# Optimization experiments

Measured on AMD Instinct MI355X. Metric: run time of the kernel, lower is better.

Reference implementation:

```python
import jax, jax.numpy as jnp
import numpy as np

N_NODES, F_IN, HID = 50000, 128, 64
N_EDGES = 400000


def _mean_agg(x, ei, n):
    # mean of src features over incoming edges per dst node
    src, dst = ei[0], ei[1]
    s = jax.ops.segment_sum(x[src], dst, num_segments=n)
    cnt = jax.ops.segment_sum(jnp.ones((ei.shape[1],), x.dtype), dst, num_segments=n)
    return s / jnp.maximum(cnt, 1.0)[:, None]


def _conv(x, ei, Wd, Ws, Wu):
    # HeteroGNNConv: mean-aggregate, then lin_dst(x_dst) || lin_src(aggr) -> lin_update
    agg = _mean_agg(x, ei, x.shape[0])
    comb = jnp.concatenate([x @ Wd.T, agg @ Ws.T], axis=-1)  # [N, 2H]
    return comb @ Wu.T


def _bn(x, g, b):
    # BatchNorm1d training-mode, eps=1 (as in the source), biased variance
    m = x.mean(axis=0)
    v = jnp.var(x, axis=0)
    return (x - m) * jax.lax.rsqrt(v + 1.0) * g + b


def setup_inputs() -> dict:
    key = jax.random.key(0)
    ks = jax.random.split(key, 20)
    d = {}
    d['node_feature'] = jax.random.normal(ks[0], (N_NODES, F_IN), dtype=jnp.float32)
    d['edge_index0'] = jax.random.randint(ks[1], (2, N_EDGES), 0, N_NODES, dtype=jnp.int32)
    d['edge_index1'] = jax.random.randint(ks[2], (2, N_EDGES), 0, N_NODES, dtype=jnp.int32)
    i = 3
    for layer, fin in (('l1', F_IN), ('l2', HID)):
        for t in ('t0', 't1'):
            d[f'{layer}{t}_Wd'] = jax.random.normal(ks[i], (HID, fin), dtype=jnp.float32) / np.sqrt(fin); i += 1
            d[f'{layer}{t}_Ws'] = jax.random.normal(ks[i], (HID, fin), dtype=jnp.float32) / np.sqrt(fin); i += 1
            d[f'{layer}{t}_Wu'] = jax.random.normal(ks[i], (HID, 2 * HID), dtype=jnp.float32) / np.sqrt(2 * HID); i += 1
    d['bn1_g'] = jnp.ones((HID,), jnp.float32)
    d['bn1_b'] = jnp.zeros((HID,), jnp.float32)
    d['bn2_g'] = jnp.ones((HID,), jnp.float32)
    d['bn2_b'] = jnp.zeros((HID,), jnp.float32)
    return d


def reference(node_feature, edge_index0, edge_index1,
              l1t0_Wd, l1t0_Ws, l1t0_Wu, l1t1_Wd, l1t1_Ws, l1t1_Wu,
              l2t0_Wd, l2t0_Ws, l2t0_Wu, l2t1_Wd, l2t1_Ws, l2t1_Wu,
              bn1_g, bn1_b, bn2_g, bn2_b):
    x = node_feature
    # layer 1: two message-type convs, mean cross-type aggregation, BN, LeakyReLU
    h = 0.5 * (_conv(x, edge_index0, l1t0_Wd, l1t0_Ws, l1t0_Wu)
               + _conv(x, edge_index1, l1t1_Wd, l1t1_Ws, l1t1_Wu))
    x = jax.nn.leaky_relu(_bn(h, bn1_g, bn1_b), negative_slope=0.01)
    # layer 2
    h = 0.5 * (_conv(x, edge_index0, l2t0_Wd, l2t0_Ws, l2t0_Wu)
               + _conv(x, edge_index1, l2t1_Wd, l2t1_Ws, l2t1_Wu))
    x = jax.nn.leaky_relu(_bn(h, bn2_g, bn2_b), negative_slope=0.01)
    # edge embeddings: [src || dst] per edge, concatenated over edge types
    e0 = jnp.concatenate([x[edge_index0[0]], x[edge_index0[1]]], axis=1)
    e1 = jnp.concatenate([x[edge_index1[0]], x[edge_index1[1]]], axis=1)
    return jnp.concatenate([e0, e1], axis=0)  # [2E, 2H]
```

## Files before the change

### kernel.cpp

```cpp
#include <hip/hip_runtime.h>
#include <math.h>


typedef float f32x4 __attribute__((ext_vector_type(4)));
typedef float f32x2 __attribute__((ext_vector_type(2)));
typedef short bf16x8 __attribute__((ext_vector_type(8)));
typedef unsigned short u16x4 __attribute__((ext_vector_type(4)));

#define NB_SCAN 64

static __device__ __forceinline__ unsigned short f2bf(float f) {
  unsigned int u = __builtin_bit_cast(unsigned int, f);
  unsigned int r = (u + 0x7FFFu + ((u >> 16) & 1u)) >> 16;
  return (unsigned short)r;
}
static __device__ __forceinline__ float bfl(unsigned int u) {
  return __builtin_bit_cast(float, u << 16);
}
static __device__ __forceinline__ float bfh(unsigned int u) {
  return __builtin_bit_cast(float, u & 0xFFFF0000u);
}

__global__ void zero_cnt(int* __restrict__ cnt0, int* __restrict__ cnt1,
                         float* __restrict__ s1, float* __restrict__ s2, int N) {
  int g = blockIdx.x * 256 + threadIdx.x;
  if (g < N) { cnt0[g] = 0; cnt1[g] = 0; }
  if (g < 256) { s1[g] = 0.f; s2[g] = 0.f; }
}

__global__ void prep_kernel(const float* __restrict__ x, unsigned short* __restrict__ xb,
                            int n4, int cvtB,
                            const float* __restrict__ Wd10, const float* __restrict__ Ws10,
                            const float* __restrict__ Wu10, const float* __restrict__ Wd11,
                            const float* __restrict__ Ws11, const float* __restrict__ Wu11,
                            unsigned short* __restrict__ Wfb1,
                            const float* __restrict__ Wd20, const float* __restrict__ Ws20,
                            const float* __restrict__ Wu20, const float* __restrict__ Wd21,
                            const float* __restrict__ Ws21, const float* __restrict__ Wu21,
                            unsigned short* __restrict__ Wfb2) {
  int b = blockIdx.x;
  if (b < cvtB) {
    int g = b * 256 + threadIdx.x;
    if (g >= n4) return;
    f32x4 v = ((const f32x4*)x)[g];
    u16x4 o;
#pragma unroll
    for (int j = 0; j < 4; ++j) o[j] = f2bf(v[j]);
    ((u16x4*)xb)[g] = o;
    return;
  }
  const float *Wd0, *Ws0, *Wu0, *Wd1, *Ws1, *Wu1;
  unsigned short* Wfb;
  int K, gid;
  if (b < cvtB + 96) {
    Wd0 = Wd10; Ws0 = Ws10; Wu0 = Wu10; Wd1 = Wd11; Ws1 = Ws11; Wu1 = Wu11;
    Wfb = Wfb1; K = 128;
    gid = (b - cvtB) * 256 + threadIdx.x;
  } else {
    Wd0 = Wd20; Ws0 = Ws20; Wu0 = Wu20; Wd1 = Wd21; Ws1 = Ws21; Wu1 = Wu21;
    Wfb = Wfb2; K = 64;
    gid = (b - cvtB - 96) * 256 + threadIdx.x;
  }
  if (gid >= 192 * K) return;
  int i = gid / K, j = gid - i * K;
  float s = 0.f;
  if (i < 64) {
#pragma unroll 4
    for (int k = 0; k < 64; ++k)
      s += Wu0[i * 128 + k] * Wd0[k * K + j] + Wu1[i * 128 + k] * Wd1[k * K + j];
  } else if (i < 128) {
    int ii = i - 64;
#pragma unroll 4
    for (int k = 0; k < 64; ++k) s += Wu0[ii * 128 + 64 + k] * Ws0[k * K + j];
  } else {
    int ii = i - 128;
#pragma unroll 4
    for (int k = 0; k < 64; ++k) s += Wu1[ii * 128 + 64 + k] * Ws1[k * K + j];
  }
  Wfb[gid] = f2bf(0.5f * s);
}

__global__ void count_both(const int* __restrict__ dst0, const int* __restrict__ dst1,
                           int* __restrict__ cnt0, int* __restrict__ cnt1, int E, int eg) {
  int b = blockIdx.x;
  bool t1 = b >= eg;
  int e = (t1 ? b - eg : b) * 256 + threadIdx.x;
  if (e >= E) return;
  if (t1) atomicAdd(&cnt1[dst1[e]], 1);
  else atomicAdd(&cnt0[dst0[e]], 1);
}

__global__ __launch_bounds__(256) void scanA(const int* __restrict__ cnt0,
                                             const int* __restrict__ cnt1,
                                             int* __restrict__ bsum, int N, int chunk) {
  int b = blockIdx.x;
  const int* cnt = (b < NB_SCAN) ? cnt0 : cnt1;
  int lb = (b < NB_SCAN) ? b : b - NB_SCAN;
  int lo = lb * chunk, hi = min(lo + chunk, N);
  int s = 0;
  for (int i = lo + threadIdx.x; i < hi; i += 256) s += cnt[i];
  __shared__ int red[256];
  red[threadIdx.x] = s;
  __syncthreads();
  for (int off = 128; off > 0; off >>= 1) {
    if (threadIdx.x < off) red[threadIdx.x] += red[threadIdx.x + off];
    __syncthreads();
  }
  if (threadIdx.x == 0) bsum[b] = red[0];
}

__global__ void scanB(const int* __restrict__ bsum, int* __restrict__ bbase) {
  __shared__ int l[2 * NB_SCAN];
  int t = threadIdx.x;
  int v0 = bsum[t];
  l[t] = v0;
  __syncthreads();
  for (int off = 1; off < NB_SCAN; off <<= 1) {
    int v = l[t];
    if ((t & (NB_SCAN - 1)) >= off) v += l[t - off];
    __syncthreads();
    l[t] = v;
    __syncthreads();
  }
  bbase[t] = l[t] - v0;
}

__global__ __launch_bounds__(256) void scanC(const int* __restrict__ cnt0,
                                             const int* __restrict__ cnt1,
                                             const int* __restrict__ bbase,
                                             int* __restrict__ base0, int* __restrict__ base1,
                                             int N, int chunk, int E) {
  int b = blockIdx.x;
  const int* cnt = (b < NB_SCAN) ? cnt0 : cnt1;
  int* base = (b < NB_SCAN) ? base0 : base1;
  int lb = (b < NB_SCAN) ? b : b - NB_SCAN;
  int lo = lb * chunk, hi = min(lo + chunk, N);
  int t = threadIdx.x;
  int v[4];
  int ls = 0;
  int i0 = lo + t * 4;
#pragma unroll
  for (int j = 0; j < 4; ++j) {
    v[j] = (i0 + j < hi) ? cnt[i0 + j] : 0;
    ls += v[j];
  }
  __shared__ int l[256];
  l[t] = ls;
  __syncthreads();
  for (int off = 1; off < 256; off <<= 1) {
    int x = l[t];
    if (t >= off) x += l[t - off];
    __syncthreads();
    l[t] = x;
    __syncthreads();
  }
  int run = bbase[b] + l[t] - ls;
#pragma unroll
  for (int j = 0; j < 4; ++j) {
    if (i0 + j < hi) base[i0 + j] = run;
    run += v[j];
  }
  if (t == 0 && lb == NB_SCAN - 1) base[N] = E;
}

__global__ void fill_both(const int* __restrict__ src0, const int* __restrict__ dst0,
                          const int* __restrict__ base0, int* __restrict__ cnt0,
                          int* __restrict__ csr0,
                          const int* __restrict__ src1, const int* __restrict__ dst1,
                          const int* __restrict__ base1, int* __restrict__ cnt1,
                          int* __restrict__ csr1, int E, int eg) {
  int b = blockIdx.x;
  bool t1 = b >= eg;
  int e = (t1 ? b - eg : b) * 256 + threadIdx.x;
  if (e >= E) return;
  const int* src = t1 ? src1 : src0;
  const int* dst = t1 ? dst1 : dst0;
  const int* base = t1 ? base1 : base0;
  int* cnt = t1 ? cnt1 : cnt0;
  int* csr = t1 ? csr1 : csr0;
  int d = dst[e];
  int p = atomicSub(&cnt[d], 1) - 1;
  csr[base[d] + p] = src[e];
}

template <int K>
__global__ __launch_bounds__(256) void mm_mfma(const unsigned short* __restrict__ xb,
                                               const unsigned short* __restrict__ Wfb,
                                               float* __restrict__ h,
                                               unsigned short* __restrict__ P0,
                                               unsigned short* __restrict__ P1, int N) {
  constexpr int NKS = K / 32;
  int tid = threadIdx.x;
  int l = tid & 63;
  int wv = tid >> 6;
  int lr = l & 15;
  int lj = l >> 4;
  int brow = blockIdx.x * 64;
  int wcol = wv * 48;

  bf16x8 B[3 * NKS];
#pragma unroll
  for (int ct = 0; ct < 3; ++ct)
#pragma unroll
    for (int ks = 0; ks < NKS; ++ks) {
      int col = wcol + ct * 16 + lr;
      B[ct * NKS + ks] = *(const bf16x8*)&Wfb[(size_t)col * K + ks * 32 + lj * 8];
    }

  f32x4 acc[4][3];
#pragma unroll
  for (int rt = 0; rt < 4; ++rt)
#pragma unroll
    for (int ct = 0; ct < 3; ++ct) acc[rt][ct] = (f32x4){0.f, 0.f, 0.f, 0.f};

#pragma unroll
  for (int ks = 0; ks < NKS; ++ks) {
    bf16x8 A[4];
#pragma unroll
    for (int rt = 0; rt < 4; ++rt) {
      int row = brow + rt * 16 + lr;
      if (row >= N) row = N - 1;
      A[rt] = *(const bf16x8*)&xb[(size_t)row * K + ks * 32 + lj * 8];
    }
#pragma unroll
    for (int rt = 0; rt < 4; ++rt)
#pragma unroll
      for (int ct = 0; ct < 3; ++ct)
        acc[rt][ct] =
            __builtin_amdgcn_mfma_f32_16x16x32_bf16(A[rt], B[ct * NKS + ks], acc[rt][ct], 0, 0, 0);
  }

#pragma unroll
  for (int rt = 0; rt < 4; ++rt)
#pragma unroll
    for (int ct = 0; ct < 3; ++ct) {
      int gct = (wcol >> 4) + ct;
      int sel = gct >> 2;
      int c0 = (gct & 3) * 16 + lr;
#pragma unroll
      for (int r = 0; r < 4; ++r) {
        int row = brow + rt * 16 + lj * 4 + r;
        if (row < N) {
          if (sel == 0) h[(size_t)row * 64 + c0] = acc[rt][ct][r];
          else if (sel == 1) P0[(size_t)row * 64 + c0] = f2bf(acc[rt][ct][r]);
          else P1[(size_t)row * 64 + c0] = f2bf(acc[rt][ct][r]);
        }
      }
    }
}

__global__ void agg_kernel(float* __restrict__ h, const unsigned short* __restrict__ P0,
                           const unsigned short* __restrict__ P1,
                           const int* __restrict__ csr0, const int* __restrict__ base0,
                           const int* __restrict__ csr1, const int* __restrict__ base1,
                           int N) {
  int gid = blockIdx.x * blockDim.x + threadIdx.x;
  int w = gid >> 5, c = gid & 31;
  if (w >= N) return;
  int co = 2 * c;
  float a0 = 0.f, a1 = 0.f;
  int b0 = base0[w], e0 = base0[w + 1];
  for (int i = b0; i < e0; ++i) {
    unsigned int u = *(const unsigned int*)&P0[(size_t)csr0[i] * 64 + co];
    a0 += bfl(u);
    a1 += bfh(u);
  }
  float i0 = 1.0f / fmaxf((float)(e0 - b0), 1.0f);
  float s0 = a0 * i0, s1 = a1 * i0;
  a0 = 0.f; a1 = 0.f;
  int b1 = base1[w], e1 = base1[w + 1];
  for (int i = b1; i < e1; ++i) {
    unsigned int u = *(const unsigned int*)&P1[(size_t)csr1[i] * 64 + co];
    a0 += bfl(u);
    a1 += bfh(u);
  }
  float i1 = 1.0f / fmaxf((float)(e1 - b1), 1.0f);
  s0 += a0 * i1;
  s1 += a1 * i1;
  f32x2* hp = (f32x2*)&h[(size_t)w * 64 + co];
  f32x2 hv = *hp;
  hv.x += s0;
  hv.y += s1;
  *hp = hv;
}

__global__ __launch_bounds__(256) void bnstats_kernel(const float* __restrict__ h,
                                                      float* __restrict__ stats, int N) {
  int tid = threadIdx.x;
  int c = tid & 63;
  int part = tid >> 6;
  float s = 0.f, s2 = 0.f;
  for (int r = blockIdx.x * 4 + part; r < N; r += gridDim.x * 4) {
    float v = h[(size_t)r * 64 + c];
    s += v;
    s2 += v * v;
  }
  __shared__ float red[512];
  red[tid] = s;
  red[256 + tid] = s2;
  __syncthreads();
  if (part == 0) {
    s = red[c] + red[64 + c] + red[128 + c] + red[192 + c];
    s2 = red[256 + c] + red[256 + 64 + c] + red[256 + 128 + c] + red[256 + 192 + c];
    atomicAdd(&stats[c], s);
    atomicAdd(&stats[64 + c], s2);
  }
}

__global__ void bnfinal_kernel(float* __restrict__ stats, const float* __restrict__ g,
                               const float* __restrict__ b, float invN) {
  int c = threadIdx.x;
  if (c >= 64) return;
  float m = stats[c] * invN;
  float v = stats[64 + c] * invN - m * m;
  float a = g[c] * rsqrtf(v + 1.0f);
  stats[128 + c] = a;
  stats[192 + c] = b[c] - m * a;
}

__global__ void bnapply_kernel(const float* __restrict__ h, const float* __restrict__ stats,
                               unsigned short* __restrict__ xo, int N) {
  int gid = blockIdx.x * blockDim.x + threadIdx.x;
  if (gid >= N * 16) return;
  f32x4 v = ((const f32x4*)h)[gid];
  int c = (gid & 15) * 4;
  const float* a = stats + 128;
  const float* bb = stats + 192;
  u16x4 o;
#pragma unroll
  for (int j = 0; j < 4; ++j) {
    float t = fmaf(a[c + j], v[j], bb[c + j]);
    o[j] = f2bf(fmaxf(t, 0.01f * t));
  }
  ((u16x4*)xo)[gid] = o;
}

__global__ void gather_kernel(const unsigned short* __restrict__ xc,
                              const int* __restrict__ src0, const int* __restrict__ dst0,
                              const int* __restrict__ src1, const int* __restrict__ dst1,
                              float* __restrict__ out, int E) {
  int gid = blockIdx.x * blockDim.x + threadIdx.x;
  int total = 2 * E * 32;
  if (gid >= total) return;
  int row = gid >> 5, q = gid & 31;
  int e, s, d;
  if (row < E) {
    e = row; s = src0[e]; d = dst0[e];
  } else {
    e = row - E; s = src1[e]; d = dst1[e];
  }
  int node = (q < 16) ? s : d;
  int qq = q & 15;
  u16x4 v = *(const u16x4*)&xc[(size_t)node * 64 + qq * 4];
  f32x4 o;
#pragma unroll
  for (int j = 0; j < 4; ++j) o[j] = bfl((unsigned int)v[j]);
  __builtin_nontemporal_store(o, (f32x4*)out + gid);
}

extern "C" void kernel_launch(void* const* d_in, const int* in_sizes, int n_in,
                              void* d_out, int out_size, void* d_ws, size_t ws_size,
                              hipStream_t stream) {
  const float* x0 = (const float*)d_in[0];
  const int* ei0 = (const int*)d_in[1];
  const int* ei1 = (const int*)d_in[2];
  const float* bn1_g = (const float*)d_in[15];
  const float* bn1_b = (const float*)d_in[16];
  const float* bn2_g = (const float*)d_in[17];
  const float* bn2_b = (const float*)d_in[18];

  const int N = in_sizes[0] / 128;
  const int E = in_sizes[1] / 2;
  const int *src0 = ei0, *dst0 = ei0 + E;
  const int *src1 = ei1, *dst1 = ei1 + E;

  char* wsb = (char*)d_ws;
  size_t off = 0;
  auto alloc = [&](size_t bytes) {
    char* p = wsb + off;
    off = (off + bytes + 255) & ~(size_t)255;
    return (void*)p;
  };
  unsigned short* Wfb1 = (unsigned short*)alloc(192 * 128 * 2);
  unsigned short* Wfb2 = (unsigned short*)alloc(192 * 64 * 2);
  float* stats1 = (float*)alloc(256 * 4);
  float* stats2 = (float*)alloc(256 * 4);
  int* bsum = (int*)alloc(2 * NB_SCAN * 4);
  int* bbase = (int*)alloc(2 * NB_SCAN * 4);
  int* cnt0 = (int*)alloc((size_t)N * 4);
  int* cnt1 = (int*)alloc((size_t)N * 4);
  int* base0 = (int*)alloc(((size_t)N + 1) * 4);
  int* base1 = (int*)alloc(((size_t)N + 1) * 4);
  int* csr0 = (int*)alloc((size_t)E * 4);
  int* csr1 = (int*)alloc((size_t)E * 4);
  unsigned short* xb = (unsigned short*)alloc((size_t)N * 128 * 2);
  float* h = (float*)alloc((size_t)N * 64 * 4);
  float* h2 = (float*)alloc((size_t)N * 64 * 4);
  unsigned short* P0 = (unsigned short*)alloc((size_t)N * 64 * 2);
  unsigned short* P1 = (unsigned short*)alloc((size_t)N * 64 * 2);
  unsigned short* xcb = (unsigned short*)alloc((size_t)N * 64 * 2);
  unsigned short* xc2 = (unsigned short*)alloc((size_t)N * 64 * 2);

  const float invN = 1.0f / (float)N;
  const int eg = (E + 255) / 256;
  const int chunk = (N + NB_SCAN - 1) / NB_SCAN;
  const int cvtB = (N * 32 + 255) / 256;

  zero_cnt<<<(N + 255) / 256, 256, 0, stream>>>(cnt0, cnt1, stats1, stats2, N);
  prep_kernel<<<cvtB + 96 + 48, 256, 0, stream>>>(
      x0, xb, N * 32, cvtB,
      (const float*)d_in[3], (const float*)d_in[4], (const float*)d_in[5],
      (const float*)d_in[6], (const float*)d_in[7], (const float*)d_in[8], Wfb1,
      (const float*)d_in[9], (const float*)d_in[10], (const float*)d_in[11],
      (const float*)d_in[12], (const float*)d_in[13], (const float*)d_in[14], Wfb2);
  count_both<<<2 * eg, 256, 0, stream>>>(dst0, dst1, cnt0, cnt1, E, eg);
  scanA<<<2 * NB_SCAN, 256, 0, stream>>>(cnt0, cnt1, bsum, N, chunk);
  scanB<<<1, 2 * NB_SCAN, 0, stream>>>(bsum, bbase);
  scanC<<<2 * NB_SCAN, 256, 0, stream>>>(cnt0, cnt1, bbase, base0, base1, N, chunk, E);
  fill_both<<<2 * eg, 256, 0, stream>>>(src0, dst0, base0, cnt0, csr0,
                                        src1, dst1, base1, cnt1, csr1, E, eg);

  const int mmGrid = (N + 63) / 64;
  const int aggGrid = (N * 32 + 255) / 256;

  mm_mfma<128><<<mmGrid, 256, 0, stream>>>(xb, Wfb1, h, P0, P1, N);
  agg_kernel<<<aggGrid, 256, 0, stream>>>(h, P0, P1, csr0, base0, csr1, base1, N);
  bnstats_kernel<<<256, 256, 0, stream>>>(h, stats1, N);
  bnfinal_kernel<<<1, 64, 0, stream>>>(stats1, bn1_g, bn1_b, invN);
  bnapply_kernel<<<(N * 16 + 255) / 256, 256, 0, stream>>>(h, stats1, xcb, N);

  mm_mfma<64><<<mmGrid, 256, 0, stream>>>(xcb, Wfb2, h2, P0, P1, N);
  agg_kernel<<<aggGrid, 256, 0, stream>>>(h2, P0, P1, csr0, base0, csr1, base1, N);
  bnstats_kernel<<<256, 256, 0, stream>>>(h2, stats2, N);
  bnfinal_kernel<<<1, 64, 0, stream>>>(stats2, bn2_g, bn2_b, invN);
  bnapply_kernel<<<(N * 16 + 255) / 256, 256, 0, stream>>>(h2, stats2, xc2, N);

  gather_kernel<<<(2 * E * 32 + 255) / 256, 256, 0, stream>>>(
      xc2, src0, dst0, src1, dst1, (float*)d_out, E);
}
```

Measured before the change: 367.6 us.

## Fuse fp32-to-bf16 conversion and BatchNorm apply into MFMA matmul loads

The first matmul now reads fp32 node features directly and converts them to bf16 in registers, which removes the separate conversion pass and the xb buffer. The second matmul applies layer-1 BatchNorm and LeakyReLU on the fly while loading its inputs, which drops the bnapply pass and the xcb buffer. The BN finalize step is folded into consumer kernels through shared memory, and count zeroing is merged into the weight-prep kernel. Together these remove several launches and full-array round trips, at the cost of wider fp32 loads and redundant per-block stat computation.

```diff
diff --git a/kernel.cpp b/kernel.cpp
--- a/kernel.cpp
+++ b/kernel.cpp
@@ -21,45 +21,34 @@
   return __builtin_bit_cast(float, u & 0xFFFF0000u);
 }
 
-__global__ void zero_cnt(int* __restrict__ cnt0, int* __restrict__ cnt1,
-                         float* __restrict__ s1, float* __restrict__ s2, int N) {
-  int g = blockIdx.x * 256 + threadIdx.x;
-  if (g < N) { cnt0[g] = 0; cnt1[g] = 0; }
-  if (g < 256) { s1[g] = 0.f; s2[g] = 0.f; }
-}
-
-__global__ void prep_kernel(const float* __restrict__ x, unsigned short* __restrict__ xb,
-                            int n4, int cvtB,
-                            const float* __restrict__ Wd10, const float* __restrict__ Ws10,
+__global__ void prep_kernel(const float* __restrict__ Wd10, const float* __restrict__ Ws10,
                             const float* __restrict__ Wu10, const float* __restrict__ Wd11,
                             const float* __restrict__ Ws11, const float* __restrict__ Wu11,
                             unsigned short* __restrict__ Wfb1,
                             const float* __restrict__ Wd20, const float* __restrict__ Ws20,
                             const float* __restrict__ Wu20, const float* __restrict__ Wd21,
                             const float* __restrict__ Ws21, const float* __restrict__ Wu21,
-                            unsigned short* __restrict__ Wfb2) {
+                            unsigned short* __restrict__ Wfb2,
+                            int* __restrict__ cnt0, int* __restrict__ cnt1,
+                            float* __restrict__ s1, float* __restrict__ s2, int N) {
   int b = blockIdx.x;
-  if (b < cvtB) {
-    int g = b * 256 + threadIdx.x;
-    if (g >= n4) return;
-    f32x4 v = ((const f32x4*)x)[g];
-    u16x4 o;
-#pragma unroll
-    for (int j = 0; j < 4; ++j) o[j] = f2bf(v[j]);
-    ((u16x4*)xb)[g] = o;
+  if (b >= 144) {
+    int g = (b - 144) * 256 + threadIdx.x;
+    if (g < N) { cnt0[g] = 0; cnt1[g] = 0; }
+    if (g < 128) { s1[g] = 0.f; s2[g] = 0.f; }
     return;
   }
   const float *Wd0, *Ws0, *Wu0, *Wd1, *Ws1, *Wu1;
   unsigned short* Wfb;
   int K, gid;
-  if (b < cvtB + 96) {
+  if (b < 96) {
     Wd0 = Wd10; Ws0 = Ws10; Wu0 = Wu10; Wd1 = Wd11; Ws1 = Ws11; Wu1 = Wu11;
     Wfb = Wfb1; K = 128;
-    gid = (b - cvtB) * 256 + threadIdx.x;
+    gid = b * 256 + threadIdx.x;
   } else {
     Wd0 = Wd20; Ws0 = Ws20; Wu0 = Wu20; Wd1 = Wd21; Ws1 = Ws21; Wu1 = Wu21;
     Wfb = Wfb2; K = 64;
-    gid = (b - cvtB - 96) * 256 + threadIdx.x;
+    gid = (b - 96) * 256 + threadIdx.x;
   }
   if (gid >= 192 * K) return;
   int i = gid / K, j = gid - i * K;
@@ -183,14 +172,28 @@
   csr[base[d] + p] = src[e];
 }
 
-template <int K>
-__global__ __launch_bounds__(256) void mm_mfma(const unsigned short* __restrict__ xb,
+template <int K, bool BN>
+__global__ __launch_bounds__(256) void mm_mfma(const float* __restrict__ xa,
                                                const unsigned short* __restrict__ Wfb,
+                                               const float* __restrict__ stats,
+                                               const float* __restrict__ gg,
+                                               const float* __restrict__ bb, float invN,
                                                float* __restrict__ h,
                                                unsigned short* __restrict__ P0,
                                                unsigned short* __restrict__ P1, int N) {
   constexpr int NKS = K / 32;
+  __shared__ float sa[64], sb[64];
   int tid = threadIdx.x;
+  if constexpr (BN) {
+    if (tid < 64) {
+      float m = stats[tid] * invN;
+      float v = stats[64 + tid] * invN - m * m;
+      float a = gg[tid] * rsqrtf(v + 1.0f);
+      sa[tid] = a;
+      sb[tid] = bb[tid] - m * a;
+    }
+    __syncthreads();
+  }
   int l = tid & 63;
   int wv = tid >> 6;
   int lr = l & 15;
@@ -215,12 +218,30 @@
 
 #pragma unroll
   for (int ks = 0; ks < NKS; ++ks) {
+    int colbase = ks * 32 + lj * 8;
     bf16x8 A[4];
 #pragma unroll
     for (int rt = 0; rt < 4; ++rt) {
       int row = brow + rt * 16 + lr;
       if (row >= N) row = N - 1;
-      A[rt] = *(const bf16x8*)&xb[(size_t)row * K + ks * 32 + lj * 8];
+      const float* p = &xa[(size_t)row * K + colbase];
+      f32x4 v0 = *(const f32x4*)p;
+      f32x4 v1 = *(const f32x4*)(p + 4);
+      bf16x8 r;
+#pragma unroll
+      for (int j = 0; j < 4; ++j) {
+        float t0 = v0[j], t1 = v1[j];
+        if constexpr (BN) {
+          int c0 = colbase + j, c1 = colbase + 4 + j;
+          t0 = fmaf(sa[c0], t0, sb[c0]);
+          t0 = fmaxf(t0, 0.01f * t0);
+          t1 = fmaf(sa[c1], t1, sb[c1]);
+          t1 = fmaxf(t1, 0.01f * t1);
+        }
+        r[j] = (short)f2bf(t0);
+        r[4 + j] = (short)f2bf(t1);
+      }
+      A[rt] = r;
     }
 #pragma unroll
     for (int rt = 0; rt < 4; ++rt)
@@ -307,29 +328,27 @@
   }
 }
 
-__global__ void bnfinal_kernel(float* __restrict__ stats, const float* __restrict__ g,
-                               const float* __restrict__ b, float invN) {
-  int c = threadIdx.x;
-  if (c >= 64) return;
-  float m = stats[c] * invN;
-  float v = stats[64 + c] * invN - m * m;
-  float a = g[c] * rsqrtf(v + 1.0f);
-  stats[128 + c] = a;
-  stats[192 + c] = b[c] - m * a;
-}
-
 __global__ void bnapply_kernel(const float* __restrict__ h, const float* __restrict__ stats,
-                               unsigned short* __restrict__ xo, int N) {
+                               const float* __restrict__ gg, const float* __restrict__ bb,
+                               float invN, unsigned short* __restrict__ xo, int N) {
+  __shared__ float sa[64], sb[64];
+  if (threadIdx.x < 64) {
+    int c = threadIdx.x;
+    float m = stats[c] * invN;
+    float v = stats[64 + c] * invN - m * m;
+    float a = gg[c] * rsqrtf(v + 1.0f);
+    sa[c] = a;
+    sb[c] = bb[c] - m * a;
+  }
+  __syncthreads();
   int gid = blockIdx.x * blockDim.x + threadIdx.x;
   if (gid >= N * 16) return;
   f32x4 v = ((const f32x4*)h)[gid];
   int c = (gid & 15) * 4;
-  const float* a = stats + 128;
-  const float* bb = stats + 192;
   u16x4 o;
 #pragma unroll
   for (int j = 0; j < 4; ++j) {
-    float t = fmaf(a[c + j], v[j], bb[c + j]);
+    float t = fmaf(sa[c + j], v[j], sb[c + j]);
     o[j] = f2bf(fmaxf(t, 0.01f * t));
   }
   ((u16x4*)xo)[gid] = o;
@@ -383,8 +402,8 @@
   };
   unsigned short* Wfb1 = (unsigned short*)alloc(192 * 128 * 2);
   unsigned short* Wfb2 = (unsigned short*)alloc(192 * 64 * 2);
-  float* stats1 = (float*)alloc(256 * 4);
-  float* stats2 = (float*)alloc(256 * 4);
+  float* stats1 = (float*)alloc(128 * 4);
+  float* stats2 = (float*)alloc(128 * 4);
   int* bsum = (int*)alloc(2 * NB_SCAN * 4);
   int* bbase = (int*)alloc(2 * NB_SCAN * 4);
   int* cnt0 = (int*)alloc((size_t)N * 4);
@@ -393,26 +412,23 @@
   int* base1 = (int*)alloc(((size_t)N + 1) * 4);
   int* csr0 = (int*)alloc((size_t)E * 4);
   int* csr1 = (int*)alloc((size_t)E * 4);
-  unsigned short* xb = (unsigned short*)alloc((size_t)N * 128 * 2);
   float* h = (float*)alloc((size_t)N * 64 * 4);
   float* h2 = (float*)alloc((size_t)N * 64 * 4);
   unsigned short* P0 = (unsigned short*)alloc((size_t)N * 64 * 2);
   unsigned short* P1 = (unsigned short*)alloc((size_t)N * 64 * 2);
-  unsigned short* xcb = (unsigned short*)alloc((size_t)N * 64 * 2);
   unsigned short* xc2 = (unsigned short*)alloc((size_t)N * 64 * 2);
 
   const float invN = 1.0f / (float)N;
   const int eg = (E + 255) / 256;
   const int chunk = (N + NB_SCAN - 1) / NB_SCAN;
-  const int cvtB = (N * 32 + 255) / 256;
-
-  zero_cnt<<<(N + 255) / 256, 256, 0, stream>>>(cnt0, cnt1, stats1, stats2, N);
-  prep_kernel<<<cvtB + 96 + 48, 256, 0, stream>>>(
-      x0, xb, N * 32, cvtB,
+  const int zb = (N + 255) / 256;
+
+  prep_kernel<<<144 + zb, 256, 0, stream>>>(
       (const float*)d_in[3], (const float*)d_in[4], (const float*)d_in[5],
       (const float*)d_in[6], (const float*)d_in[7], (const float*)d_in[8], Wfb1,
       (const float*)d_in[9], (const float*)d_in[10], (const float*)d_in[11],
-      (const float*)d_in[12], (const float*)d_in[13], (const float*)d_in[14], Wfb2);
+      (const float*)d_in[12], (const float*)d_in[13], (const float*)d_in[14], Wfb2,
+      cnt0, cnt1, stats1, stats2, N);
   count_both<<<2 * eg, 256, 0, stream>>>(dst0, dst1, cnt0, cnt1, E, eg);
   scanA<<<2 * NB_SCAN, 256, 0, stream>>>(cnt0, cnt1, bsum, N, chunk);
   scanB<<<1, 2 * NB_SCAN, 0, stream>>>(bsum, bbase);
@@ -423,17 +439,17 @@
   const int mmGrid = (N + 63) / 64;
   const int aggGrid = (N * 32 + 255) / 256;
 
-  mm_mfma<128><<<mmGrid, 256, 0, stream>>>(xb, Wfb1, h, P0, P1, N);
+  mm_mfma<128, false><<<mmGrid, 256, 0, stream>>>(x0, Wfb1, nullptr, nullptr, nullptr, 0.f,
+                                                  h, P0, P1, N);
   agg_kernel<<<aggGrid, 256, 0, stream>>>(h, P0, P1, csr0, base0, csr1, base1, N);
   bnstats_kernel<<<256, 256, 0, stream>>>(h, stats1, N);
-  bnfinal_kernel<<<1, 64, 0, stream>>>(stats1, bn1_g, bn1_b, invN);
-  bnapply_kernel<<<(N * 16 + 255) / 256, 256, 0, stream>>>(h, stats1, xcb, N);
-
-  mm_mfma<64><<<mmGrid, 256, 0, stream>>>(xcb, Wfb2, h2, P0, P1, N);
+
+  mm_mfma<64, true><<<mmGrid, 256, 0, stream>>>(h, Wfb2, stats1, bn1_g, bn1_b, invN,
+                                                h2, P0, P1, N);
   agg_kernel<<<aggGrid, 256, 0, stream>>>(h2, P0, P1, csr0, base0, csr1, base1, N);
   bnstats_kernel<<<256, 256, 0, stream>>>(h2, stats2, N);
-  bnfinal_kernel<<<1, 64, 0, stream>>>(stats2, bn2_g, bn2_b, invN);
-  bnapply_kernel<<<(N * 16 + 255) / 256, 256, 0, stream>>>(h2, stats2, xc2, N);
+  bnapply_kernel<<<(N * 16 + 255) / 256, 256, 0, stream>>>(h2, stats2, bn2_g, bn2_b, invN,
+                                                           xc2, N);
 
   gather_kernel<<<(2 * E * 32 + 255) / 256, 256, 0, stream>>>(
       xc2, src0, dst0, src1, dst1, (float*)d_out, E);
```

Result: no change. 365.5 us (-0.6%).
